# Performance work log

Measured on AMD Instinct MI355X. Metric: run time of the kernel, lower is better.

Reference implementation:

```python
import jax, jax.numpy as jnp
import numpy as np

N = 500_000
B = 10_000
D = 256
H = 256
NODES_PER_GRAPH = N // B
BN_EPS = 1e-5


def setup_inputs() -> dict:
    key = jax.random.key(0)
    ks = jax.random.split(key, 8)
    s = 1.0 / np.sqrt(D)
    feat = jax.random.normal(ks[0], (N, D), dtype=jnp.float32)
    intend = jax.random.normal(ks[1], (B, D), dtype=jnp.float32)
    # B graphs of equal size; sorted segment ids, last node of each graph
    segment_ids = jnp.repeat(jnp.arange(B, dtype=jnp.int32), NODES_PER_GRAPH)
    last_nodes = (jnp.arange(B, dtype=jnp.int32) + 1) * NODES_PER_GRAPH - 1
    return {
        "feat": feat,
        "intend": intend,
        "last_nodes": last_nodes,
        "segment_ids": segment_ids,
        "W_u": jax.random.uniform(ks[2], (D, H), jnp.float32, -s, s),
        "W_v": jax.random.uniform(ks[3], (D, H), jnp.float32, -s, s),
        "b_v": jnp.zeros((H,), jnp.float32),
        "W_i": jax.random.uniform(ks[4], (D, H), jnp.float32, -s, s),
        "b_i": jnp.zeros((H,), jnp.float32),
        "W_e": jax.random.uniform(ks[5], (H, 1), jnp.float32, -1.0 / np.sqrt(H), 1.0 / np.sqrt(H)),
        "bn_gamma": jnp.ones((D,), jnp.float32),
        "bn_beta": jnp.zeros((D,), jnp.float32),
        "bn_mean": jnp.zeros((D,), jnp.float32),
        "bn_var": jnp.ones((D,), jnp.float32),
    }


def reference(feat, intend, last_nodes, segment_ids, W_u, W_v, b_v, W_i, b_i, W_e,
              bn_gamma, bn_beta, bn_mean, bn_var):
    num_graphs = intend.shape[0]
    # BatchNorm1d in eval mode (running stats)
    feat = (feat - bn_mean) * (bn_gamma / jnp.sqrt(bn_var + BN_EPS)) + bn_beta
    # dropout p=0.0 -> identity
    feat_u = feat @ W_u                                   # [N, H]
    last_emb = feat[last_nodes] @ W_i + b_i               # [B, H]
    feat_v = intend @ W_v + b_v                           # [B, H]
    per_graph = last_emb + feat_v                         # [B, H]
    # broadcast_nodes: gather per-graph vectors to nodes
    gate = jax.nn.sigmoid(feat_u + per_graph[segment_ids])  # [N, H]
    e = (gate @ W_e)[:, 0]                                # [N]
    # ragged segment softmax
    m = jax.ops.segment_max(e, segment_ids, num_segments=num_graphs)
    ex = jnp.exp(e - m[segment_ids])
    denom = jax.ops.segment_sum(ex, segment_ids, num_segments=num_graphs)
    alpha = ex / denom[segment_ids]                       # [N]
    # weighted segment-sum readout
    rst = jax.ops.segment_sum(feat * alpha[:, None], segment_ids, num_segments=num_graphs)
    # output_dim == input_dim -> fc_out is None; activation is None
    return rst
```

## Files before the change

### kernel.cpp

```cpp
#include <hip/hip_runtime.h>
#include <hip/hip_bf16.h>
#include <stdint.h>

typedef short short8 __attribute__((ext_vector_type(8)));
typedef float f32x4 __attribute__((ext_vector_type(4)));

#define NPG   50
#define GPB   2
#define ROWS  100
#define MP    112
#define MT    7
#define LDA   264
#define NTILES 5000
#define MAIN_GRID 512
#define BN_EPS 1e-5f

__device__ __forceinline__ float bf2f(unsigned short u) {
    union { unsigned int i; float f; } v; v.i = ((unsigned int)u) << 16; return v.f;
}
__device__ __forceinline__ unsigned short f2bf(float f) {
    union { float f; unsigned int i; } v; v.f = f;
    unsigned int i = v.i;
    return (unsigned short)((i + 0x7FFFu + ((i >> 16) & 1u)) >> 16);
}
__device__ __forceinline__ unsigned int pack_bf16(float a, float b) {
    __hip_bfloat162 h = __float22bfloat162_rn(make_float2(a, b));
    unsigned int o; __builtin_memcpy(&o, &h, 4); return o;
}

__global__ __launch_bounds__(256) void prep_kernel(
    const float* __restrict__ Wu, const float* __restrict__ Wv,
    const float* __restrict__ Wi, const float* __restrict__ bi,
    const float* __restrict__ bv,
    const float* __restrict__ gamma, const float* __restrict__ beta,
    const float* __restrict__ mean, const float* __restrict__ var,
    float* __restrict__ sc, float* __restrict__ sh, float* __restrict__ gt,
    unsigned short* __restrict__ Wt, unsigned short* __restrict__ Wt2) {
    __shared__ float r4[4];
    if (blockIdx.x < 256) {
        int k = blockIdx.x, n = threadIdx.x;
        float s = gamma[k] * rsqrtf(var[k] + BN_EPS);
        Wt [n * 256 + k]       = f2bf(s * Wu[k * 256 + n]);
        Wt2[n * 512 + k]       = f2bf(s * Wi[k * 256 + n]);
        Wt2[n * 512 + 256 + k] = f2bf(Wv[k * 256 + n]);
        if (k == 0) {
            float sn = gamma[n] * rsqrtf(var[n] + BN_EPS);
            sc[n] = sn;
            sh[n] = beta[n] - mean[n] * sn;
        }
    } else {
        int n = blockIdx.x - 256, k = threadIdx.x;
        float s = gamma[k] * rsqrtf(var[k] + BN_EPS);
        float shk = beta[k] - mean[k] * s;
        float p = shk * (Wu[k * 256 + n] + Wi[k * 256 + n]);
#pragma unroll
        for (int mask = 1; mask < 64; mask <<= 1) p += __shfl_xor(p, mask, 64);
        if ((k & 63) == 0) r4[k >> 6] = p;
        __syncthreads();
        if (k == 0) gt[n] = r4[0] + r4[1] + r4[2] + r4[3] + bi[n] + bv[n];
    }
}

__global__ __launch_bounds__(256) void pgraph_kernel(
    const float* __restrict__ feat,
    const float* __restrict__ intend,
    const int* __restrict__ last_nodes,
    const unsigned short* __restrict__ Wt2,
    const float* __restrict__ gt,
    unsigned short* __restrict__ Pb, int Bnum) {
    __shared__ unsigned short A2[64 * 520];

    int tid = threadIdx.x;
    int g0 = blockIdx.x * 64;
    int k0 = (tid & 31) * 8;

    for (int t = tid; t < 64 * 32; t += 256) {
        int row = t >> 5;
        int g = g0 + row; if (g > Bnum - 1) g = Bnum - 1;
        int ln = last_nodes[g];
        const float* src = feat + (size_t)ln * 256 + k0;
        float4 u0 = *(const float4*)(src);
        float4 u1 = *(const float4*)(src + 4);
        *(uint4*)(&A2[row * 520 + k0]) = make_uint4(
            pack_bf16(u0.x, u0.y), pack_bf16(u0.z, u0.w),
            pack_bf16(u1.x, u1.y), pack_bf16(u1.z, u1.w));
    }
    for (int t = tid; t < 64 * 32; t += 256) {
        int row = t >> 5;
        int g = g0 + row; if (g > Bnum - 1) g = Bnum - 1;
        const float* src = intend + (size_t)g * 256 + k0;
        float4 u0 = *(const float4*)(src);
        float4 u1 = *(const float4*)(src + 4);
        *(uint4*)(&A2[row * 520 + 256 + k0]) = make_uint4(
            pack_bf16(u0.x, u0.y), pack_bf16(u0.z, u0.w),
            pack_bf16(u1.x, u1.y), pack_bf16(u1.z, u1.w));
    }
    __syncthreads();

    int w = tid >> 6, l = tid & 63, lm = l & 15, lq = l >> 4;
    int nbase = w * 64;
    float bias4[4];
#pragma unroll
    for (int nt = 0; nt < 4; ++nt) bias4[nt] = gt[nbase + nt*16 + lm];

    for (int mt = 0; mt < 4; ++mt) {
        f32x4 acc[4];
#pragma unroll
        for (int nt = 0; nt < 4; ++nt) acc[nt] = (f32x4){0.f, 0.f, 0.f, 0.f};
#pragma unroll
        for (int ks = 0; ks < 16; ++ks) {
            short8 a = *(const short8*)(&A2[(mt*16 + lm) * 520 + ks*32 + lq*8]);
#pragma unroll
            for (int nt = 0; nt < 4; ++nt) {
                short8 b = *(const short8*)(Wt2 + (size_t)(nbase + nt*16 + lm) * 512 + ks*32 + lq*8);
                acc[nt] = __builtin_amdgcn_mfma_f32_16x16x32_bf16(a, b, acc[nt], 0, 0, 0);
            }
        }
#pragma unroll
        for (int nt = 0; nt < 4; ++nt) {
            int col = nbase + nt*16 + lm;
#pragma unroll
            for (int r = 0; r < 4; ++r) {
                int row = mt*16 + lq*4 + r;
                int g = g0 + row;
                if (g < Bnum) Pb[(size_t)g * 256 + col] = f2bf(acc[nt][r] + bias4[nt]);
            }
        }
    }
}

__global__ __launch_bounds__(256, 2) void main_kernel(
    const float* __restrict__ feat,
    const unsigned short* __restrict__ Wt,
    const float* __restrict__ We,
    const float* __restrict__ sc, const float* __restrict__ sh,
    const unsigned short* __restrict__ Pb,
    float* __restrict__ out) {
    __shared__ unsigned short featA[MP * LDA];
    __shared__ float P_lds[GPB][256];
    __shared__ float e_parts[4][MP];
    __shared__ float alpha_lds[ROWS];

    int tid = threadIdx.x;
    int w = tid >> 6, l = tid & 63, lm = l & 15, lq = l >> 4;
    int nbase = w * 64;

    short8 bfr[4][8];
#pragma unroll
    for (int nt = 0; nt < 4; ++nt)
#pragma unroll
        for (int ks = 0; ks < 8; ++ks)
            bfr[nt][ks] = *(const short8*)(Wt + (size_t)(nbase + nt*16 + lm) * 256 + ks*32 + lq*8);
    float we4[4];
#pragma unroll
    for (int nt = 0; nt < 4; ++nt) we4[nt] = We[nbase + nt*16 + lm];

    int ct = tid & 127, half = tid >> 7;
    float2 scp = *(const float2*)(sc + 2 * ct);
    float2 shp = *(const float2*)(sh + 2 * ct);

    for (int t = tid; t < (MP - ROWS) * 32; t += 256) {
        int row = ROWS + (t >> 5);
        int c0 = (t & 31) * 8;
        *(uint4*)(&featA[row * LDA + c0]) = make_uint4(0u, 0u, 0u, 0u);
    }

    for (int tile = blockIdx.x; tile < NTILES; tile += MAIN_GRID) {
        size_t row0 = (size_t)tile * ROWS;

        for (int t = tid; t < ROWS * 32; t += 256) {
            int row = t >> 5;
            int c0 = (t & 31) * 8;
            const float* src = feat + (row0 + row) * 256 + c0;
            float4 u0 = *(const float4*)(src);
            float4 u1 = *(const float4*)(src + 4);
            *(uint4*)(&featA[row * LDA + c0]) = make_uint4(
                pack_bf16(u0.x, u0.y), pack_bf16(u0.z, u0.w),
                pack_bf16(u1.x, u1.y), pack_bf16(u1.z, u1.w));
        }
        for (int t = tid; t < GPB * 256; t += 256)
            ((float*)P_lds)[t] = bf2f(Pb[(size_t)tile * GPB * 256 + t]);
        __syncthreads();

        for (int mt = 0; mt < MT; ++mt) {
            f32x4 acc[4];
#pragma unroll
            for (int nt = 0; nt < 4; ++nt) acc[nt] = (f32x4){0.f, 0.f, 0.f, 0.f};
#pragma unroll
            for (int ks = 0; ks < 8; ++ks) {
                short8 a = *(const short8*)(&featA[(mt*16 + lm) * LDA + ks*32 + lq*8]);
#pragma unroll
                for (int nt = 0; nt < 4; ++nt)
                    acc[nt] = __builtin_amdgcn_mfma_f32_16x16x32_bf16(a, bfr[nt][ks], acc[nt], 0, 0, 0);
            }
            float er[4] = {0.f, 0.f, 0.f, 0.f};
#pragma unroll
            for (int nt = 0; nt < 4; ++nt) {
                int col = nbase + nt*16 + lm;
                float pw = we4[nt];
#pragma unroll
                for (int r = 0; r < 4; ++r) {
                    int row = mt*16 + lq*4 + r;
                    int lg = (row >= NPG) ? 1 : 0;
                    float g = acc[nt][r] + P_lds[lg][col];
                    float s = __builtin_amdgcn_rcpf(1.0f + __expf(-g));
                    er[r] += s * pw;
                }
            }
#pragma unroll
            for (int r = 0; r < 4; ++r)
#pragma unroll
                for (int mask = 1; mask < 16; mask <<= 1)
                    er[r] += __shfl_xor(er[r], mask, 64);
            if (lm == 0) {
#pragma unroll
                for (int r = 0; r < 4; ++r)
                    e_parts[w][mt*16 + lq*4 + r] = er[r];
            }
        }
        __syncthreads();

        if (w < GPB) {
            float ev = -3.0e38f;
            if (l < NPG) {
                int row = w * NPG + l;
                ev = e_parts[0][row] + e_parts[1][row] + e_parts[2][row] + e_parts[3][row];
            }
            float m = ev;
#pragma unroll
            for (int mask = 1; mask < 64; mask <<= 1) m = fmaxf(m, __shfl_xor(m, mask, 64));
            float p = (l < NPG) ? __expf(ev - m) : 0.f;
            float s = p;
#pragma unroll
            for (int mask = 1; mask < 64; mask <<= 1) s += __shfl_xor(s, mask, 64);
            if (l < NPG) alpha_lds[w * NPG + l] = p * __builtin_amdgcn_rcpf(s);
        }
        __syncthreads();

        {
            float acc0 = 0.f, acc1 = 0.f;
            int colb = ct * 2;
            int rbase = half * NPG;
#pragma unroll 5
            for (int i = 0; i < NPG; i += 2) {
                int r0 = rbase + i, r1 = r0 + 1;
                float al0 = alpha_lds[r0], al1 = alpha_lds[r1];
                unsigned int u0 = *(const unsigned int*)(&featA[r0 * LDA + colb]);
                unsigned int u1 = *(const unsigned int*)(&featA[r1 * LDA + colb]);
                acc0 += al0 * bf2f((unsigned short)(u0 & 0xFFFFu))
                      + al1 * bf2f((unsigned short)(u1 & 0xFFFFu));
                acc1 += al0 * bf2f((unsigned short)(u0 >> 16))
                      + al1 * bf2f((unsigned short)(u1 >> 16));
            }
            float2 o = make_float2(scp.x * acc0 + shp.x, scp.y * acc1 + shp.y);
            *(float2*)(out + (size_t)(tile * GPB + half) * 256 + colb) = o;
        }
        __syncthreads();
    }
}

extern "C" void kernel_launch(void* const* d_in, const int* in_sizes, int n_in,
                              void* d_out, int out_size, void* d_ws, size_t ws_size,
                              hipStream_t stream) {
    const float* feat      = (const float*)d_in[0];
    const float* intend    = (const float*)d_in[1];
    const int* last_nodes  = (const int*)d_in[2];
    const float* Wu    = (const float*)d_in[4];
    const float* Wv    = (const float*)d_in[5];
    const float* bv    = (const float*)d_in[6];
    const float* Wi    = (const float*)d_in[7];
    const float* bi    = (const float*)d_in[8];
    const float* We    = (const float*)d_in[9];
    const float* gamma = (const float*)d_in[10];
    const float* beta  = (const float*)d_in[11];
    const float* mean  = (const float*)d_in[12];
    const float* var   = (const float*)d_in[13];

    int Bnum = in_sizes[2];

    char* ws = (char*)d_ws;
    float* sc = (float*)ws;
    float* sh = (float*)(ws + 1024);
    float* gt = (float*)(ws + 2048);
    unsigned short* Wt  = (unsigned short*)(ws + 4096);
    unsigned short* Wt2 = (unsigned short*)(ws + 4096 + 131072);
    unsigned short* Pb  = (unsigned short*)(ws + 4096 + 131072 + 262144);

    prep_kernel<<<512, 256, 0, stream>>>(Wu, Wv, Wi, bi, bv, gamma, beta, mean, var,
                                         sc, sh, gt, Wt, Wt2);
    pgraph_kernel<<<(Bnum + 63) / 64, 256, 0, stream>>>(feat, intend, last_nodes, Wt2,
                                                        gt, Pb, Bnum);
    main_kernel<<<MAIN_GRID, 256, 0, stream>>>(feat, Wt, We, sc, sh, Pb, (float*)d_out);
}
```

Measured before the change: 795.5 us.

## Double-buffer feature tiles with register prefetch and 512-thread contiguous tile blocks

The main kernel now runs 512 threads (8 waves, each holding 32 output columns of W_u) and gives each of 250 blocks a contiguous run of 20 tiles. The next tile's fp32 features are loaded into registers while the current tile's MFMA and softmax run, then packed into a second LDS buffer, so global load latency overlaps compute. The cost is twice the LDS per block (about 120 KB, which may allow only one block per CU despite launch_bounds(512,2)), more registers for the prefetch, and half the threads idle during the readout.

```diff
diff --git a/kernel.cpp b/kernel.cpp
--- a/kernel.cpp
+++ b/kernel.cpp
@@ -12,7 +12,8 @@
 #define MT    7
 #define LDA   264
 #define NTILES 5000
-#define MAIN_GRID 512
+#define MAIN_GRID 250
+#define TPB_TILES 20
 #define BN_EPS 1e-5f
 
 __device__ __forceinline__ float bf2f(unsigned short u) {
@@ -129,80 +130,107 @@
     }
 }
 
-__global__ __launch_bounds__(256, 2) void main_kernel(
+__global__ __launch_bounds__(512, 2) void main_kernel(
     const float* __restrict__ feat,
     const unsigned short* __restrict__ Wt,
     const float* __restrict__ We,
     const float* __restrict__ sc, const float* __restrict__ sh,
     const unsigned short* __restrict__ Pb,
     float* __restrict__ out) {
-    __shared__ unsigned short featA[MP * LDA];
-    __shared__ float P_lds[GPB][256];
-    __shared__ float e_parts[4][MP];
+    __shared__ unsigned short featA[2][MP * LDA];
+    __shared__ float P_lds[2][GPB][256];
+    __shared__ float e_parts[8][MP];
     __shared__ float alpha_lds[ROWS];
 
     int tid = threadIdx.x;
     int w = tid >> 6, l = tid & 63, lm = l & 15, lq = l >> 4;
-    int nbase = w * 64;
-
-    short8 bfr[4][8];
-#pragma unroll
-    for (int nt = 0; nt < 4; ++nt)
+    int nbase = w * 32;
+
+    short8 bfr[2][8];
+#pragma unroll
+    for (int nt = 0; nt < 2; ++nt)
 #pragma unroll
         for (int ks = 0; ks < 8; ++ks)
             bfr[nt][ks] = *(const short8*)(Wt + (size_t)(nbase + nt*16 + lm) * 256 + ks*32 + lq*8);
-    float we4[4];
-#pragma unroll
-    for (int nt = 0; nt < 4; ++nt) we4[nt] = We[nbase + nt*16 + lm];
-
-    int ct = tid & 127, half = tid >> 7;
+    float we2[2];
+#pragma unroll
+    for (int nt = 0; nt < 2; ++nt) we2[nt] = We[nbase + nt*16 + lm];
+
+    int ct = tid & 127, half = (tid >> 7) & 1;
     float2 scp = *(const float2*)(sc + 2 * ct);
     float2 shp = *(const float2*)(sh + 2 * ct);
 
-    for (int t = tid; t < (MP - ROWS) * 32; t += 256) {
-        int row = ROWS + (t >> 5);
-        int c0 = (t & 31) * 8;
-        *(uint4*)(&featA[row * LDA + c0]) = make_uint4(0u, 0u, 0u, 0u);
-    }
-
-    for (int tile = blockIdx.x; tile < NTILES; tile += MAIN_GRID) {
-        size_t row0 = (size_t)tile * ROWS;
-
-        for (int t = tid; t < ROWS * 32; t += 256) {
-            int row = t >> 5;
-            int c0 = (t & 31) * 8;
-            const float* src = feat + (row0 + row) * 256 + c0;
-            float4 u0 = *(const float4*)(src);
-            float4 u1 = *(const float4*)(src + 4);
-            *(uint4*)(&featA[row * LDA + c0]) = make_uint4(
-                pack_bf16(u0.x, u0.y), pack_bf16(u0.z, u0.w),
-                pack_bf16(u1.x, u1.y), pack_bf16(u1.z, u1.w));
-        }
-        for (int t = tid; t < GPB * 256; t += 256)
-            ((float*)P_lds)[t] = bf2f(Pb[(size_t)tile * GPB * 256 + t]);
-        __syncthreads();
+#pragma unroll
+    for (int b = 0; b < 2; ++b)
+        if (tid < (MP - ROWS) * 32) {
+            int row = ROWS + (tid >> 5), c0 = (tid & 31) * 8;
+            *(uint4*)(&featA[b][row * LDA + c0]) = make_uint4(0u, 0u, 0u, 0u);
+        }
+
+    int t0 = blockIdx.x * TPB_TILES;
+    float4 ldA[7], ldB[7];
+
+#pragma unroll
+    for (int i = 0; i < 7; ++i) {
+        int c = tid + i * 512;
+        if (c < ROWS * 32) {
+            int row = c >> 5, c0 = (c & 31) * 8;
+            const float* src = feat + ((size_t)t0 * ROWS + row) * 256 + c0;
+            ldA[i] = *(const float4*)(src);
+            ldB[i] = *(const float4*)(src + 4);
+        }
+    }
+    P_lds[0][tid >> 8][tid & 255] = bf2f(Pb[(size_t)t0 * (GPB * 256) + tid]);
+#pragma unroll
+    for (int i = 0; i < 7; ++i) {
+        int c = tid + i * 512;
+        if (c < ROWS * 32) {
+            int row = c >> 5, c0 = (c & 31) * 8;
+            *(uint4*)(&featA[0][row * LDA + c0]) = make_uint4(
+                pack_bf16(ldA[i].x, ldA[i].y), pack_bf16(ldA[i].z, ldA[i].w),
+                pack_bf16(ldB[i].x, ldB[i].y), pack_bf16(ldB[i].z, ldB[i].w));
+        }
+    }
+    __syncthreads();
+
+    for (int t = 0; t < TPB_TILES; ++t) {
+        int cb = t & 1, nb = cb ^ 1;
+        size_t tl = (size_t)(t0 + t);
+        bool hn = (t + 1 < TPB_TILES);
+
+        if (hn) {
+#pragma unroll
+            for (int i = 0; i < 7; ++i) {
+                int c = tid + i * 512;
+                if (c < ROWS * 32) {
+                    int row = c >> 5, c0 = (c & 31) * 8;
+                    const float* src = feat + ((tl + 1) * ROWS + row) * 256 + c0;
+                    ldA[i] = *(const float4*)(src);
+                    ldB[i] = *(const float4*)(src + 4);
+                }
+            }
+        }
 
         for (int mt = 0; mt < MT; ++mt) {
-            f32x4 acc[4];
-#pragma unroll
-            for (int nt = 0; nt < 4; ++nt) acc[nt] = (f32x4){0.f, 0.f, 0.f, 0.f};
+            f32x4 acc[2];
+            acc[0] = (f32x4){0.f, 0.f, 0.f, 0.f};
+            acc[1] = (f32x4){0.f, 0.f, 0.f, 0.f};
 #pragma unroll
             for (int ks = 0; ks < 8; ++ks) {
-                short8 a = *(const short8*)(&featA[(mt*16 + lm) * LDA + ks*32 + lq*8]);
-#pragma unroll
-                for (int nt = 0; nt < 4; ++nt)
-                    acc[nt] = __builtin_amdgcn_mfma_f32_16x16x32_bf16(a, bfr[nt][ks], acc[nt], 0, 0, 0);
+                short8 a = *(const short8*)(&featA[cb][(mt*16 + lm) * LDA + ks*32 + lq*8]);
+                acc[0] = __builtin_amdgcn_mfma_f32_16x16x32_bf16(a, bfr[0][ks], acc[0], 0, 0, 0);
+                acc[1] = __builtin_amdgcn_mfma_f32_16x16x32_bf16(a, bfr[1][ks], acc[1], 0, 0, 0);
             }
             float er[4] = {0.f, 0.f, 0.f, 0.f};
 #pragma unroll
-            for (int nt = 0; nt < 4; ++nt) {
+            for (int nt = 0; nt < 2; ++nt) {
                 int col = nbase + nt*16 + lm;
-                float pw = we4[nt];
+                float pw = we2[nt];
 #pragma unroll
                 for (int r = 0; r < 4; ++r) {
                     int row = mt*16 + lq*4 + r;
                     int lg = (row >= NPG) ? 1 : 0;
-                    float g = acc[nt][r] + P_lds[lg][col];
+                    float g = acc[nt][r] + P_lds[cb][lg][col];
                     float s = __builtin_amdgcn_rcpf(1.0f + __expf(-g));
                     er[r] += s * pw;
                 }
@@ -224,7 +252,9 @@
             float ev = -3.0e38f;
             if (l < NPG) {
                 int row = w * NPG + l;
-                ev = e_parts[0][row] + e_parts[1][row] + e_parts[2][row] + e_parts[3][row];
+                ev = 0.f;
+#pragma unroll
+                for (int j = 0; j < 8; ++j) ev += e_parts[j][row];
             }
             float m = ev;
 #pragma unroll
@@ -237,23 +267,37 @@
         }
         __syncthreads();
 
-        {
+        if (hn) {
+            P_lds[nb][tid >> 8][tid & 255] = bf2f(Pb[(tl + 1) * (GPB * 256) + tid]);
+#pragma unroll
+            for (int i = 0; i < 7; ++i) {
+                int c = tid + i * 512;
+                if (c < ROWS * 32) {
+                    int row = c >> 5, c0 = (c & 31) * 8;
+                    *(uint4*)(&featA[nb][row * LDA + c0]) = make_uint4(
+                        pack_bf16(ldA[i].x, ldA[i].y), pack_bf16(ldA[i].z, ldA[i].w),
+                        pack_bf16(ldB[i].x, ldB[i].y), pack_bf16(ldB[i].z, ldB[i].w));
+                }
+            }
+        }
+
+        if (tid < 256) {
             float acc0 = 0.f, acc1 = 0.f;
             int colb = ct * 2;
             int rbase = half * NPG;
 #pragma unroll 5
-            for (int i = 0; i < NPG; i += 2) {
-                int r0 = rbase + i, r1 = r0 + 1;
+            for (int i2 = 0; i2 < NPG; i2 += 2) {
+                int r0 = rbase + i2, r1 = r0 + 1;
                 float al0 = alpha_lds[r0], al1 = alpha_lds[r1];
-                unsigned int u0 = *(const unsigned int*)(&featA[r0 * LDA + colb]);
-                unsigned int u1 = *(const unsigned int*)(&featA[r1 * LDA + colb]);
+                unsigned int u0 = *(const unsigned int*)(&featA[cb][r0 * LDA + colb]);
+                unsigned int u1 = *(const unsigned int*)(&featA[cb][r1 * LDA + colb]);
                 acc0 += al0 * bf2f((unsigned short)(u0 & 0xFFFFu))
                       + al1 * bf2f((unsigned short)(u1 & 0xFFFFu));
                 acc1 += al0 * bf2f((unsigned short)(u0 >> 16))
                       + al1 * bf2f((unsigned short)(u1 >> 16));
             }
             float2 o = make_float2(scp.x * acc0 + shp.x, scp.y * acc1 + shp.y);
-            *(float2*)(out + (size_t)(tile * GPB + half) * 256 + colb) = o;
+            *(float2*)(out + ((size_t)tl * GPB + half) * 256 + colb) = o;
         }
         __syncthreads();
     }
@@ -290,5 +334,5 @@
                                          sc, sh, gt, Wt, Wt2);
     pgraph_kernel<<<(Bnum + 63) / 64, 256, 0, stream>>>(feat, intend, last_nodes, Wt2,
                                                         gt, Pb, Bnum);
-    main_kernel<<<MAIN_GRID, 256, 0, stream>>>(feat, Wt, We, sc, sh, Pb, (float*)d_out);
-}
+    main_kernel<<<MAIN_GRID, 512, 0, stream>>>(feat, Wt, We, sc, sh, Pb, (float*)d_out);
+}
```

After: 800.3 us. No clear change (+0.6%).
